# Kernel optimization log

Measured on AMD Instinct MI355X. Metric: run time of the kernel, lower is better.

The kernel has to match this reference:

```python
import jax, jax.numpy as jnp
import numpy as np

B, T = 512, 64
STOCH, DETER, HIDDEN = 32, 512, 512
ACT_DIM, EMBED = 12, 1024
MIN_STD = 0.1
LN_EPS = 1e-3


def _ln(x, g, b):
    m = x.mean(-1, keepdims=True)
    v = ((x - m) ** 2).mean(-1, keepdims=True)
    return (x - m) / jnp.sqrt(v + LN_EPS) * g + b


def setup_inputs() -> dict:
    key = jax.random.key(0)
    ks = jax.random.split(key, 12)

    def w(k, shape):
        fan_in = shape[0]
        return jax.random.normal(k, shape, jnp.float32) / np.sqrt(fan_in)

    is_first = jnp.zeros((B, T), jnp.float32).at[:, 0].set(1.0)
    return {
        "embed": jax.random.normal(ks[0], (B, T, EMBED), jnp.float32),
        "action": jax.random.normal(ks[1], (B, T, ACT_DIM), jnp.float32),
        "is_first": is_first,
        "eps_prior": jax.random.normal(ks[2], (B, T, STOCH), jnp.float32),
        "eps_post": jax.random.normal(ks[3], (B, T, STOCH), jnp.float32),
        "W_init": jax.random.normal(ks[4], (1, DETER), jnp.float32) * 0.02,
        "w_in": w(ks[5], (STOCH + ACT_DIM, HIDDEN)),
        "ln_in_g": jnp.ones((HIDDEN,), jnp.float32),
        "ln_in_b": jnp.zeros((HIDDEN,), jnp.float32),
        "w_gru": w(ks[6], (HIDDEN + DETER, 3 * DETER)),
        "ln_gru_g": jnp.ones((3 * DETER,), jnp.float32),
        "ln_gru_b": jnp.zeros((3 * DETER,), jnp.float32),
        "w_out": w(ks[7], (DETER, HIDDEN)),
        "ln_out_g": jnp.ones((HIDDEN,), jnp.float32),
        "ln_out_b": jnp.zeros((HIDDEN,), jnp.float32),
        "w_ims": w(ks[8], (HIDDEN, 2 * STOCH)),
        "b_ims": jnp.zeros((2 * STOCH,), jnp.float32),
        "w_obs": w(ks[9], (DETER + EMBED, HIDDEN)),
        "ln_obs_g": jnp.ones((HIDDEN,), jnp.float32),
        "ln_obs_b": jnp.zeros((HIDDEN,), jnp.float32),
        "w_ostat": w(ks[10], (HIDDEN, 2 * STOCH)),
        "b_ostat": jnp.zeros((2 * STOCH,), jnp.float32),
    }


def reference(embed, action, is_first, eps_prior, eps_post, W_init,
              w_in, ln_in_g, ln_in_b, w_gru, ln_gru_g, ln_gru_b,
              w_out, ln_out_g, ln_out_b, w_ims, b_ims,
              w_obs, ln_obs_g, ln_obs_b, w_ostat, b_ostat):
    # RSSM.observe with continuous stoch (discrete=False), mean_act='none',
    # std_act='softplus', initial='learned', rec_depth=1.
    def img_out_stats(deter):
        x = jax.nn.silu(_ln(deter @ w_out, ln_out_g, ln_out_b))
        s = x @ w_ims + b_ims
        mean = s[..., :STOCH]
        std = jax.nn.softplus(s[..., STOCH:]) + MIN_STD
        return mean, std

    bsz = embed.shape[0]
    deter0 = jnp.broadcast_to(jnp.tanh(W_init), (bsz, DETER))
    stoch0, _ = img_out_stats(deter0)  # mode of Normal = mean

    # time-major for scan
    eT = jnp.swapaxes(embed, 0, 1)
    aT = jnp.swapaxes(action, 0, 1)
    fT = jnp.swapaxes(is_first, 0, 1)[..., None]
    epT = jnp.swapaxes(eps_prior, 0, 1)
    eoT = jnp.swapaxes(eps_post, 0, 1)

    def step(carry, xs):
        stoch, deter = carry
        a, e, f, ep, eo = xs
        # is_first reset (blend with learned initial state)
        a = a * (1.0 - f)
        stoch = stoch * (1.0 - f) + stoch0 * f
        deter = deter * (1.0 - f) + deter0 * f
        # img_step
        x = jax.nn.silu(_ln(jnp.concatenate([stoch, a], -1) @ w_in, ln_in_g, ln_in_b))
        parts = _ln(jnp.concatenate([x, deter], -1) @ w_gru, ln_gru_g, ln_gru_b)
        r, c, u = jnp.split(parts, 3, -1)
        r = jax.nn.sigmoid(r)
        c = jnp.tanh(r * c)
        u = jax.nn.sigmoid(u - 1.0)  # update_bias = -1
        deter_n = u * c + (1.0 - u) * deter
        pm, ps = img_out_stats(deter_n)
        pstoch = pm + ps * ep  # reparameterized sample
        # obs_step posterior
        xo = jax.nn.silu(_ln(jnp.concatenate([deter_n, e], -1) @ w_obs, ln_obs_g, ln_obs_b))
        so = xo @ w_ostat + b_ostat
        om = so[..., :STOCH]
        ostd = jax.nn.softplus(so[..., STOCH:]) + MIN_STD
        ostoch = om + ostd * eo
        return (ostoch, deter_n), (ostoch, om, ostd, pstoch, pm, ps, deter_n)

    _, ys = jax.lax.scan(step, (stoch0, deter0), (aT, eT, fT, epT, eoT))
    # batch-major, concat post(stoch,mean,std) prior(stoch,mean,std) deter -> [B,T,6*STOCH+DETER]
    return jnp.concatenate([jnp.swapaxes(y, 0, 1) for y in ys], -1)
```

## Files before the change

### kernel.cpp

```cpp
#include <hip/hip_runtime.h>
#include <hip/hip_bf16.h>


typedef __attribute__((ext_vector_type(8))) short bf16x8;
typedef __attribute__((ext_vector_type(4))) float f32x4;

static __device__ __forceinline__ short f2b(float x){
  __hip_bfloat16 h = __float2bfloat16(x);
  return *reinterpret_cast<short*>(&h);
}
static __device__ __forceinline__ float b2f(short s){
  __hip_bfloat16 h = *reinterpret_cast<__hip_bfloat16*>(&s);
  return __bfloat162float(h);
}
static __device__ __forceinline__ float softplusf_(float x){
  return (x > 20.f) ? x : log1pf(expf(x));
}

static __device__ __forceinline__ float bsum(float v, float* red){
  int tid = threadIdx.x;
  __syncthreads();
  red[tid] = v; __syncthreads();
  for(int s = blockDim.x>>1; s>0; s>>=1){
    if(tid < s) red[tid] += red[tid+s];
    __syncthreads();
  }
  return red[0];
}

static __device__ __forceinline__ void stage8f(short* dst, const float* src){
  float4 f0 = *reinterpret_cast<const float4*>(src);
  float4 f1 = *reinterpret_cast<const float4*>(src+4);
  bf16x8 v;
  v[0]=f2b(f0.x); v[1]=f2b(f0.y); v[2]=f2b(f0.z); v[3]=f2b(f0.w);
  v[4]=f2b(f1.x); v[5]=f2b(f1.y); v[6]=f2b(f1.z); v[7]=f2b(f1.w);
  *reinterpret_cast<bf16x8*>(dst) = v;
}

__global__ __launch_bounds__(256) void k_wt(const float* __restrict__ wg,
    const float* __restrict__ wo, const float* __restrict__ wou,
    short* __restrict__ wgruT, short* __restrict__ wobsDT,
    short* __restrict__ wobsET, short* __restrict__ woutT){
  int i = blockIdx.x*256 + threadIdx.x;
  if(i < 1572864){ int n = i>>10, k = i&1023; wgruT[i] = f2b(wg[k*1536+n]); return; }
  i -= 1572864;
  if(i < 262144){ int n = i>>9, k = i&511; wobsDT[i] = f2b(wo[k*512+n]); return; }
  i -= 262144;
  if(i < 524288){ int n = i>>10, k = i&1023; wobsET[i] = f2b(wo[(512+k)*512+n]); return; }
  i -= 524288;
  { int n = i>>9, k = i&511; woutT[i] = f2b(wou[k*512+n]); }
}

__global__ __launch_bounds__(512) void k_init(const float* __restrict__ W_init,
    const float* __restrict__ w_out, const float* __restrict__ og, const float* __restrict__ ob,
    const float* __restrict__ w_ims, const float* __restrict__ b_ims,
    float* __restrict__ deter0, float* __restrict__ stoch0){
  __shared__ float d0[512]; __shared__ float red[512]; __shared__ float x2[512];
  int tid = threadIdx.x;
  float d = tanhf(W_init[tid]); d0[tid] = d; deter0[tid] = d; __syncthreads();
  float s = 0.f;
  for(int k=0;k<512;k++) s += d0[k]*w_out[k*512+tid];
  float sum = bsum(s, red);
  float sq  = bsum(s*s, red);
  float mu = sum/512.f, var = sq/512.f - mu*mu;
  float rstd = rsqrtf(var + 1e-3f);
  float xn = (s-mu)*rstd*og[tid] + ob[tid];
  float xs = xn/(1.f+expf(-xn));
  x2[tid] = xs; __syncthreads();
  if(tid < 32){
    float acc = b_ims[tid];
    for(int k=0;k<512;k++) acc += x2[k]*w_ims[k*64+tid];
    stoch0[tid] = acc;
  }
}

__global__ __launch_bounds__(256) void k_x0(const float* __restrict__ action,
    const float* __restrict__ is_first, const float* __restrict__ w_in,
    const float* __restrict__ ig, const float* __restrict__ ib,
    const float* __restrict__ deter0, const float* __restrict__ stoch0,
    short* __restrict__ xdeter, float* __restrict__ deterF){
  int b = blockIdx.x, tid = threadIdx.x;
  __shared__ float st[32]; __shared__ float al[12]; __shared__ float red[256];
  float f0 = is_first[b*64];
  if(tid < 32) st[tid] = stoch0[tid];
  if(tid < 12) al[tid] = action[b*768 + tid]*(1.f-f0);
  __syncthreads();
  float xp[2];
  for(int i=0;i<2;i++){
    int h = tid + i*256; float a = 0.f;
    for(int k=0;k<32;k++) a += st[k]*w_in[k*512+h];
    for(int k=0;k<12;k++) a += al[k]*w_in[(32+k)*512+h];
    xp[i] = a;
  }
  float sum = bsum(xp[0]+xp[1], red);
  float sq  = bsum(xp[0]*xp[0]+xp[1]*xp[1], red);
  float mu = sum/512.f, var = sq/512.f - mu*mu;
  float rstd = rsqrtf(var + 1e-3f);
  for(int i=0;i<2;i++){
    int h = tid + i*256;
    float xn = (xp[i]-mu)*rstd*ig[h]+ib[h];
    float xs = xn/(1.f+expf(-xn));
    xdeter[b*1024 + h] = f2b(xs);
    xdeter[b*1024 + 512 + h] = f2b(deter0[h]);
    deterF[b*512 + h] = deter0[h];
  }
}

__global__ __launch_bounds__(256) void k_gru(const short* __restrict__ Axd,
    const short* __restrict__ Bw, float* __restrict__ Cp){
  __shared__ __align__(16) short As[64][72];
  __shared__ __align__(16) short Bs[64][72];
  int tid = threadIdx.x, lane = tid&63, wid = tid>>6;
  int wm = (wid>>1)*32, wn = (wid&1)*32;
  int mP = blockIdx.x*64, nP = blockIdx.y*64;
  f32x4 acc[2][2] = {};
  for(int kt=0; kt<1024; kt+=64){
    #pragma unroll
    for(int c=0;c<2;c++){
      int idx = tid + c*256; int r = idx>>3, kc = (idx&7)*8;
      *(int4*)&As[r][kc] = *(const int4*)&Axd[(mP+r)*1024 + kt + kc];
      *(int4*)&Bs[r][kc] = *(const int4*)&Bw[(nP+r)*1024 + kt + kc];
    }
    __syncthreads();
    #pragma unroll
    for(int ks=0; ks<64; ks+=32){
      int ko = ks + 8*(lane>>4);
      bf16x8 a0 = *(const bf16x8*)&As[wm +      (lane&15)][ko];
      bf16x8 a1 = *(const bf16x8*)&As[wm + 16 + (lane&15)][ko];
      bf16x8 b0 = *(const bf16x8*)&Bs[wn +      (lane&15)][ko];
      bf16x8 b1 = *(const bf16x8*)&Bs[wn + 16 + (lane&15)][ko];
      acc[0][0] = __builtin_amdgcn_mfma_f32_16x16x32_bf16(a0,b0,acc[0][0],0,0,0);
      acc[0][1] = __builtin_amdgcn_mfma_f32_16x16x32_bf16(a0,b1,acc[0][1],0,0,0);
      acc[1][0] = __builtin_amdgcn_mfma_f32_16x16x32_bf16(a1,b0,acc[1][0],0,0,0);
      acc[1][1] = __builtin_amdgcn_mfma_f32_16x16x32_bf16(a1,b1,acc[1][1],0,0,0);
    }
    __syncthreads();
  }
  int r0 = (lane>>4)*4, c0 = lane&15;
  for(int mi=0;mi<2;mi++) for(int ni=0;ni<2;ni++){
    int row = mP + wm + mi*16 + r0, col = nP + wn + ni*16 + c0;
    #pragma unroll
    for(int r=0;r<4;r++) Cp[(row+r)*1536 + col] = acc[mi][ni][r];
  }
}

__global__ __launch_bounds__(256) void k_gates(const float* __restrict__ parts,
    const float* __restrict__ gg, const float* __restrict__ gb,
    const float* __restrict__ is_first, const float* __restrict__ deter0,
    float* __restrict__ deterF, short* __restrict__ deterB,
    float* __restrict__ out, int t){
  int b = blockIdx.x, tid = threadIdx.x;
  __shared__ float red[256];
  const float* p = parts + b*1536;
  float v[6]; float s=0.f, sq=0.f;
  #pragma unroll
  for(int k=0;k<6;k++){ v[k] = p[tid + k*256]; s += v[k]; sq += v[k]*v[k]; }
  float sum = bsum(s, red);
  float ssq = bsum(sq, red);
  float mu = sum/1536.f, var = ssq/1536.f - mu*mu;
  float rstd = rsqrtf(var + 1e-3f);
  float f = is_first[b*64 + t];
  for(int jj=0;jj<2;jj++){
    int j = tid + jj*256;
    float xr = (v[jj]  -mu)*rstd*gg[j]       + gb[j];
    float xc = (v[2+jj]-mu)*rstd*gg[512+j]   + gb[512+j];
    float xu = (v[4+jj]-mu)*rstd*gg[1024+j]  + gb[1024+j];
    float r = 1.f/(1.f+expf(-xr));
    float c = tanhf(r*xc);
    float u = 1.f/(1.f+expf(-(xu-1.f)));
    float dp = deterF[b*512+j]*(1.f-f) + deter0[j]*f;
    float dn = u*c + (1.f-u)*dp;
    deterF[b*512+j] = dn;
    deterB[b*512+j] = f2b(dn);
    out[b*45056 + t*704 + 192 + j] = dn;
  }
}

__global__ __launch_bounds__(256) void k_obs(const short* __restrict__ dB,
    const float* __restrict__ emb, const short* __restrict__ WdT,
    const short* __restrict__ WeT, float* __restrict__ xopre, int t){
  __shared__ __align__(16) short As[64][72];
  __shared__ __align__(16) short Bs[64][72];
  int tid = threadIdx.x, lane = tid&63, wid = tid>>6;
  int wm = (wid>>1)*32, wn = (wid&1)*32;
  int mP = blockIdx.x*64, nP = blockIdx.y*64;
  f32x4 acc[2][2] = {};
  for(int kt=0; kt<24; kt++){
    #pragma unroll
    for(int c=0;c<2;c++){
      int idx = tid + c*256; int r = idx>>3, kc = (idx&7)*8;
      if(kt < 8){
        *(int4*)&As[r][kc] = *(const int4*)&dB[(mP+r)*512 + kt*64 + kc];
        *(int4*)&Bs[r][kc] = *(const int4*)&WdT[(nP+r)*512 + kt*64 + kc];
      } else {
        stage8f(&As[r][kc], &emb[(mP+r)*65536 + t*1024 + (kt-8)*64 + kc]);
        *(int4*)&Bs[r][kc] = *(const int4*)&WeT[(nP+r)*1024 + (kt-8)*64 + kc];
      }
    }
    __syncthreads();
    #pragma unroll
    for(int ks=0; ks<64; ks+=32){
      int ko = ks + 8*(lane>>4);
      bf16x8 a0 = *(const bf16x8*)&As[wm +      (lane&15)][ko];
      bf16x8 a1 = *(const bf16x8*)&As[wm + 16 + (lane&15)][ko];
      bf16x8 b0 = *(const bf16x8*)&Bs[wn +      (lane&15)][ko];
      bf16x8 b1 = *(const bf16x8*)&Bs[wn + 16 + (lane&15)][ko];
      acc[0][0] = __builtin_amdgcn_mfma_f32_16x16x32_bf16(a0,b0,acc[0][0],0,0,0);
      acc[0][1] = __builtin_amdgcn_mfma_f32_16x16x32_bf16(a0,b1,acc[0][1],0,0,0);
      acc[1][0] = __builtin_amdgcn_mfma_f32_16x16x32_bf16(a1,b0,acc[1][0],0,0,0);
      acc[1][1] = __builtin_amdgcn_mfma_f32_16x16x32_bf16(a1,b1,acc[1][1],0,0,0);
    }
    __syncthreads();
  }
  int r0 = (lane>>4)*4, c0 = lane&15;
  for(int mi=0;mi<2;mi++) for(int ni=0;ni<2;ni++){
    int row = mP + wm + mi*16 + r0, col = nP + wn + ni*16 + c0;
    #pragma unroll
    for(int r=0;r<4;r++) xopre[(row+r)*512 + col] = acc[mi][ni][r];
  }
}

__global__ __launch_bounds__(256) void k_post(const float* __restrict__ xopre,
    const float* __restrict__ og, const float* __restrict__ ob,
    const float* __restrict__ w_ostat, const float* __restrict__ b_ostat,
    const float* __restrict__ eps_post, const float* __restrict__ is_first,
    const float* __restrict__ action, const float* __restrict__ w_in,
    const float* __restrict__ ig, const float* __restrict__ ib,
    const float* __restrict__ stoch0, const float* __restrict__ deter0,
    const float* __restrict__ deterF, short* __restrict__ xdeter,
    float* __restrict__ out, int t){
  int b = blockIdx.x, tid = threadIdx.x;
  __shared__ float red[256]; __shared__ float xo[512];
  __shared__ float psh[4][64]; __shared__ float sol[64];
  __shared__ float st[32]; __shared__ float al[12];
  float xv[2];
  for(int i=0;i<2;i++) xv[i] = xopre[b*512 + tid + i*256];
  float sum = bsum(xv[0]+xv[1], red);
  float sq  = bsum(xv[0]*xv[0]+xv[1]*xv[1], red);
  float mu = sum/512.f, var = sq/512.f - mu*mu;
  float rstd = rsqrtf(var + 1e-3f);
  for(int i=0;i<2;i++){
    int h = tid + i*256;
    float xn = (xv[i]-mu)*rstd*og[h]+ob[h];
    xo[h] = xn/(1.f+expf(-xn));
  }
  __syncthreads();
  { int p = tid>>6, n = tid&63; float a = 0.f;
    for(int k=p*128; k<p*128+128; k++) a += xo[k]*w_ostat[k*64+n];
    psh[p][n] = a; }
  __syncthreads();
  if(tid < 64) sol[tid] = psh[0][tid]+psh[1][tid]+psh[2][tid]+psh[3][tid] + b_ostat[tid];
  __syncthreads();
  float fn = (t < 63) ? is_first[b*64 + t + 1] : 0.f;
  if(tid < 32){
    float om = sol[tid];
    float osd = softplusf_(sol[32+tid]) + 0.1f;
    float eo = eps_post[(b*64+t)*32 + tid];
    float ost = om + osd*eo;
    int base = b*45056 + t*704;
    out[base+tid] = ost; out[base+32+tid] = om; out[base+64+tid] = osd;
    st[tid] = ost*(1.f-fn) + stoch0[tid]*fn;
  }
  if(tid < 12 && t < 63) al[tid] = action[(b*64+t+1)*12 + tid]*(1.f-fn);
  __syncthreads();
  if(t < 63){
    float xp[2];
    for(int i=0;i<2;i++){
      int h = tid + i*256; float a = 0.f;
      for(int k=0;k<32;k++) a += st[k]*w_in[k*512+h];
      for(int k=0;k<12;k++) a += al[k]*w_in[(32+k)*512+h];
      xp[i] = a;
    }
    float s2 = bsum(xp[0]+xp[1], red);
    float q2 = bsum(xp[0]*xp[0]+xp[1]*xp[1], red);
    float mu2 = s2/512.f, var2 = q2/512.f - mu2*mu2;
    float rstd2 = rsqrtf(var2 + 1e-3f);
    for(int i=0;i<2;i++){
      int h = tid + i*256;
      float xn = (xp[i]-mu2)*rstd2*ig[h]+ib[h];
      float xs = xn/(1.f+expf(-xn));
      xdeter[b*1024 + h] = f2b(xs);
      xdeter[b*1024 + 512 + h] = f2b(deterF[b*512+h]*(1.f-fn) + deter0[h]*fn);
    }
  }
}

__global__ __launch_bounds__(256) void k_img(const float* __restrict__ outp,
    const short* __restrict__ WoT, short* __restrict__ x2pre){
  __shared__ __align__(16) short As[128][72];
  __shared__ __align__(16) short Bs[128][72];
  int tid = threadIdx.x, lane = tid&63, wid = tid>>6;
  int wm = (wid>>1)*64, wn = (wid&1)*64;
  int mP = blockIdx.x*128, nP = blockIdx.y*128;
  f32x4 acc[4][4] = {};
  for(int kt=0; kt<512; kt+=64){
    #pragma unroll
    for(int c=0;c<4;c++){
      int idx = tid + c*256; int r = idx>>3, kc = (idx&7)*8;
      stage8f(&As[r][kc], &outp[(mP+r)*704 + 192 + kt + kc]);
      *(int4*)&Bs[r][kc] = *(const int4*)&WoT[(nP+r)*512 + kt + kc];
    }
    __syncthreads();
    #pragma unroll
    for(int ks=0; ks<64; ks+=32){
      int ko = ks + 8*(lane>>4);
      bf16x8 a[4], b[4];
      #pragma unroll
      for(int i=0;i<4;i++){
        a[i] = *(const bf16x8*)&As[wm + i*16 + (lane&15)][ko];
        b[i] = *(const bf16x8*)&Bs[wn + i*16 + (lane&15)][ko];
      }
      #pragma unroll
      for(int mi=0;mi<4;mi++)
        #pragma unroll
        for(int ni=0;ni<4;ni++)
          acc[mi][ni] = __builtin_amdgcn_mfma_f32_16x16x32_bf16(a[mi],b[ni],acc[mi][ni],0,0,0);
    }
    __syncthreads();
  }
  int r0 = (lane>>4)*4, c0 = lane&15;
  for(int mi=0;mi<4;mi++) for(int ni=0;ni<4;ni++){
    int row = mP + wm + mi*16 + r0, col = nP + wn + ni*16 + c0;
    #pragma unroll
    for(int r=0;r<4;r++) x2pre[(row+r)*512 + col] = f2b(acc[mi][ni][r]);
  }
}

__global__ __launch_bounds__(256) void k_imgpost(const short* __restrict__ x2pre,
    const float* __restrict__ og, const float* __restrict__ ob,
    const float* __restrict__ w_ims, const float* __restrict__ b_ims,
    const float* __restrict__ eps_prior, float* __restrict__ out){
  int tid = threadIdx.x;
  int g = tid>>5, l = tid&31;
  int rbase = blockIdx.x*8;
  __shared__ float x2[8][512]; __shared__ float sl[8][64];
  int row = rbase + g;
  float vals[16]; float s=0.f, sq=0.f;
  #pragma unroll
  for(int i=0;i<16;i++){
    int k = l + i*32;
    float v = b2f(x2pre[row*512+k]);
    vals[i] = v; s += v; sq += v*v;
  }
  #pragma unroll
  for(int m=1;m<32;m<<=1){ s += __shfl_xor(s, m); sq += __shfl_xor(sq, m); }
  float mu = s/512.f, var = sq/512.f - mu*mu;
  float rstd = rsqrtf(var + 1e-3f);
  #pragma unroll
  for(int i=0;i<16;i++){
    int k = l + i*32;
    float xn = (vals[i]-mu)*rstd*og[k]+ob[k];
    x2[g][k] = xn/(1.f+expf(-xn));
  }
  __syncthreads();
  { int q = tid>>6, n = tid&63;
    float a0=0.f, a1=0.f;
    for(int k=0;k<512;k++){
      float w = w_ims[k*64+n];
      a0 += x2[q][k]*w; a1 += x2[q+4][k]*w;
    }
    sl[q][n]=a0; sl[q+4][n]=a1; }
  __syncthreads();
  { int r = tid>>5, n = tid&31; int rw = rbase + r;
    float pm = sl[r][n] + b_ims[n];
    float psd = softplusf_(sl[r][n+32] + b_ims[n+32]) + 0.1f;
    float ep = eps_prior[rw*32+n];
    int base = rw*704;
    out[base+96+n] = pm + psd*ep; out[base+128+n] = pm; out[base+160+n] = psd; }
}

extern "C" void kernel_launch(void* const* d_in, const int* in_sizes, int n_in,
                              void* d_out, int out_size, void* d_ws, size_t ws_size,
                              hipStream_t stream) {
  const float* embed     = (const float*)d_in[0];
  const float* action    = (const float*)d_in[1];
  const float* is_first  = (const float*)d_in[2];
  const float* eps_prior = (const float*)d_in[3];
  const float* eps_post  = (const float*)d_in[4];
  const float* W_init    = (const float*)d_in[5];
  const float* w_in      = (const float*)d_in[6];
  const float* ln_in_g   = (const float*)d_in[7];
  const float* ln_in_b   = (const float*)d_in[8];
  const float* w_gru     = (const float*)d_in[9];
  const float* ln_gru_g  = (const float*)d_in[10];
  const float* ln_gru_b  = (const float*)d_in[11];
  const float* w_out     = (const float*)d_in[12];
  const float* ln_out_g  = (const float*)d_in[13];
  const float* ln_out_b  = (const float*)d_in[14];
  const float* w_ims     = (const float*)d_in[15];
  const float* b_ims     = (const float*)d_in[16];
  const float* w_obs     = (const float*)d_in[17];
  const float* ln_obs_g  = (const float*)d_in[18];
  const float* ln_obs_b  = (const float*)d_in[19];
  const float* w_ostat   = (const float*)d_in[20];
  const float* b_ostat   = (const float*)d_in[21];
  float* out = (float*)d_out;
  char* ws = (char*)d_ws;

  short* wgruT  = (short*)(ws + 0);
  short* wobsDT = (short*)(ws + 3145728);
  short* wobsET = (short*)(ws + 3670016);
  short* woutT  = (short*)(ws + 4718592);
  float* deter0 = (float*)(ws + 5242880);
  float* stoch0 = (float*)(ws + 5244928);
  short* xdeter = (short*)(ws + 5245184);
  float* parts  = (float*)(ws + 6293760);
  float* deterF = (float*)(ws + 9439488);
  short* deterB = (short*)(ws + 10488064);
  float* xopre  = (float*)(ws + 11012352);
  short* x2pre  = (short*)(ws + 12060928);

  dim3 blk(256);
  hipLaunchKernelGGL(k_wt, dim3(10240), blk, 0, stream,
                     w_gru, w_obs, w_out, wgruT, wobsDT, wobsET, woutT);
  hipLaunchKernelGGL(k_init, dim3(1), dim3(512), 0, stream,
                     W_init, w_out, ln_out_g, ln_out_b, w_ims, b_ims, deter0, stoch0);
  hipLaunchKernelGGL(k_x0, dim3(512), blk, 0, stream,
                     action, is_first, w_in, ln_in_g, ln_in_b, deter0, stoch0, xdeter, deterF);
  for(int t=0; t<64; t++){
    hipLaunchKernelGGL(k_gru, dim3(8,24), blk, 0, stream, xdeter, wgruT, parts);
    hipLaunchKernelGGL(k_gates, dim3(512), blk, 0, stream,
                       parts, ln_gru_g, ln_gru_b, is_first, deter0, deterF, deterB, out, t);
    hipLaunchKernelGGL(k_obs, dim3(8,8), blk, 0, stream,
                       deterB, embed, wobsDT, wobsET, xopre, t);
    hipLaunchKernelGGL(k_post, dim3(512), blk, 0, stream,
                       xopre, ln_obs_g, ln_obs_b, w_ostat, b_ostat, eps_post, is_first,
                       action, w_in, ln_in_g, ln_in_b, stoch0, deter0, deterF, xdeter, out, t);
  }
  hipLaunchKernelGGL(k_img, dim3(256,4), blk, 0, stream, out, woutT, x2pre);
  hipLaunchKernelGGL(k_imgpost, dim3(4096), blk, 0, stream,
                     x2pre, ln_out_g, ln_out_b, w_ims, b_ims, eps_prior, out);
}
```

Baseline: 5.789 ms.

## Fuse the whole recurrent scan into one persistent kernel with fragment-swizzled weights

The 64-step loop of four kernels per step (GRU GEMM, gates, obs GEMM, posterior plus next input) becomes one persistent kernel. It runs 32 blocks of 1024 threads, and each block owns 16 batch rows across all timesteps, keeping deter, stoch and intermediates in LDS. The input, GRU, obs and ostat weights are pre-transposed into bf16 MFMA fragment order so each wave can load B fragments straight from global memory. Layer-norm statistics use wave shuffles plus LDS atomics. The aim is to remove per-step launch overhead and the global round trips of intermediates. In exchange only 32 CUs are used, and every block re-streams several MB of weights from cache each step. Some pre-norm intermediates are also rounded to bf16.

```diff
diff --git a/kernel.cpp b/kernel.cpp
--- a/kernel.cpp
+++ b/kernel.cpp
@@ -16,39 +16,45 @@
 static __device__ __forceinline__ float softplusf_(float x){
   return (x > 20.f) ? x : log1pf(expf(x));
 }
-
-static __device__ __forceinline__ float bsum(float v, float* red){
-  int tid = threadIdx.x;
-  __syncthreads();
-  red[tid] = v; __syncthreads();
-  for(int s = blockDim.x>>1; s>0; s>>=1){
-    if(tid < s) red[tid] += red[tid+s];
-    __syncthreads();
-  }
-  return red[0];
-}
-
-static __device__ __forceinline__ void stage8f(short* dst, const float* src){
-  float4 f0 = *reinterpret_cast<const float4*>(src);
-  float4 f1 = *reinterpret_cast<const float4*>(src+4);
-  bf16x8 v;
-  v[0]=f2b(f0.x); v[1]=f2b(f0.y); v[2]=f2b(f0.z); v[3]=f2b(f0.w);
-  v[4]=f2b(f1.x); v[5]=f2b(f1.y); v[6]=f2b(f1.z); v[7]=f2b(f1.w);
-  *reinterpret_cast<bf16x8*>(dst) = v;
-}
-
-__global__ __launch_bounds__(256) void k_wt(const float* __restrict__ wg,
-    const float* __restrict__ wo, const float* __restrict__ wou,
-    short* __restrict__ wgruT, short* __restrict__ wobsDT,
-    short* __restrict__ wobsET, short* __restrict__ woutT){
+static __device__ __forceinline__ float sigm(float x){ return 1.f/(1.f+expf(-x)); }
+
+__global__ __launch_bounds__(256) void k_wt(
+    const float* __restrict__ wi, const float* __restrict__ wg,
+    const float* __restrict__ wo, const float* __restrict__ wst,
+    const float* __restrict__ wou,
+    short* __restrict__ WinT, short* __restrict__ WgruT,
+    short* __restrict__ WobsT, short* __restrict__ WostatT,
+    short* __restrict__ WoutT){
   int i = blockIdx.x*256 + threadIdx.x;
-  if(i < 1572864){ int n = i>>10, k = i&1023; wgruT[i] = f2b(wg[k*1536+n]); return; }
+  if(i < 32768){
+    int e=i&7, l=(i>>3)&63, f=i>>9; int ks=f&1, nt=f>>1;
+    int k=ks*32+((l>>4))*8+e, n=nt*16+(l&15);
+    WinT[i] = (k<44)? f2b(wi[k*512+n]) : (short)0;
+    return;
+  }
+  i -= 32768;
+  if(i < 1572864){
+    int e=i&7, l=(i>>3)&63, f=i>>9; int ks=f&31, nt=f>>5;
+    int k=ks*32+((l>>4))*8+e, n=nt*16+(l&15);
+    WgruT[i] = f2b(wg[k*1536+n]);
+    return;
+  }
   i -= 1572864;
-  if(i < 262144){ int n = i>>9, k = i&511; wobsDT[i] = f2b(wo[k*512+n]); return; }
-  i -= 262144;
-  if(i < 524288){ int n = i>>10, k = i&1023; wobsET[i] = f2b(wo[(512+k)*512+n]); return; }
-  i -= 524288;
-  { int n = i>>9, k = i&511; woutT[i] = f2b(wou[k*512+n]); }
+  if(i < 786432){
+    int e=i&7, l=(i>>3)&63, f=i>>9; int ks=f%48, nt=f/48;
+    int k=ks*32+((l>>4))*8+e, n=nt*16+(l&15);
+    WobsT[i] = f2b(wo[k*512+n]);
+    return;
+  }
+  i -= 786432;
+  if(i < 32768){
+    int e=i&7, l=(i>>3)&63, f=i>>9; int ks=f&15, nt=f>>4;
+    int k=ks*32+((l>>4))*8+e, n=nt*16+(l&15);
+    WostatT[i] = f2b(wst[k*64+n]);
+    return;
+  }
+  i -= 32768;
+  { int n=i>>9, k=i&511; WoutT[i] = f2b(wou[k*512+n]); }
 }
 
 __global__ __launch_bounds__(512) void k_init(const float* __restrict__ W_init,
@@ -60,12 +66,16 @@
   float d = tanhf(W_init[tid]); d0[tid] = d; deter0[tid] = d; __syncthreads();
   float s = 0.f;
   for(int k=0;k<512;k++) s += d0[k]*w_out[k*512+tid];
-  float sum = bsum(s, red);
-  float sq  = bsum(s*s, red);
+  red[tid] = s; __syncthreads();
+  for(int ss=256; ss>0; ss>>=1){ if(tid<ss) red[tid]+=red[tid+ss]; __syncthreads(); }
+  float sum = red[0]; __syncthreads();
+  red[tid] = s*s; __syncthreads();
+  for(int ss=256; ss>0; ss>>=1){ if(tid<ss) red[tid]+=red[tid+ss]; __syncthreads(); }
+  float sq = red[0];
   float mu = sum/512.f, var = sq/512.f - mu*mu;
   float rstd = rsqrtf(var + 1e-3f);
   float xn = (s-mu)*rstd*og[tid] + ob[tid];
-  float xs = xn/(1.f+expf(-xn));
+  float xs = xn*sigm(xn);
   x2[tid] = xs; __syncthreads();
   if(tid < 32){
     float acc = b_ims[tid];
@@ -74,214 +84,257 @@
   }
 }
 
-__global__ __launch_bounds__(256) void k_x0(const float* __restrict__ action,
-    const float* __restrict__ is_first, const float* __restrict__ w_in,
-    const float* __restrict__ ig, const float* __restrict__ ib,
+__global__ __launch_bounds__(1024, 4) void k_scan(
+    const float* __restrict__ embed, const float* __restrict__ action,
+    const float* __restrict__ isf, const float* __restrict__ eps_post,
+    const short* __restrict__ WinT, const float* __restrict__ ig, const float* __restrict__ ib,
+    const short* __restrict__ WgruT, const float* __restrict__ gg, const float* __restrict__ gb,
+    const short* __restrict__ WobsT, const float* __restrict__ og, const float* __restrict__ ob,
+    const short* __restrict__ WostatT, const float* __restrict__ b_ostat,
     const float* __restrict__ deter0, const float* __restrict__ stoch0,
-    short* __restrict__ xdeter, float* __restrict__ deterF){
-  int b = blockIdx.x, tid = threadIdx.x;
-  __shared__ float st[32]; __shared__ float al[12]; __shared__ float red[256];
-  float f0 = is_first[b*64];
-  if(tid < 32) st[tid] = stoch0[tid];
-  if(tid < 12) al[tid] = action[b*768 + tid]*(1.f-f0);
+    float* __restrict__ out)
+{
+  __shared__ __align__(16) short RB[16*1544];
+  __shared__ float deterS[16][516];
+  __shared__ short dB[16][520];
+  __shared__ short xrow[16][72];
+  __shared__ float stochS[16][32];
+  __shared__ float sol[16][64];
+  __shared__ float sumA[16], sqA[16];
+  __shared__ float fr[16];
+  __shared__ float d0s[512]; __shared__ float s0s[32];
+
+  const int g = blockIdx.x, tid = threadIdx.x;
+  const int w = tid>>6, lane = tid&63;
+  const int col0 = lane&15, rg4 = (lane>>4)*4;
+  float* xoF = (float*)RB;
+
+  if(tid < 512) d0s[tid] = deter0[tid];
+  if(tid < 32)  s0s[tid] = stoch0[tid];
   __syncthreads();
-  float xp[2];
-  for(int i=0;i<2;i++){
-    int h = tid + i*256; float a = 0.f;
-    for(int k=0;k<32;k++) a += st[k]*w_in[k*512+h];
-    for(int k=0;k<12;k++) a += al[k]*w_in[(32+k)*512+h];
-    xp[i] = a;
-  }
-  float sum = bsum(xp[0]+xp[1], red);
-  float sq  = bsum(xp[0]*xp[0]+xp[1]*xp[1], red);
-  float mu = sum/512.f, var = sq/512.f - mu*mu;
-  float rstd = rsqrtf(var + 1e-3f);
-  for(int i=0;i<2;i++){
-    int h = tid + i*256;
-    float xn = (xp[i]-mu)*rstd*ig[h]+ib[h];
-    float xs = xn/(1.f+expf(-xn));
-    xdeter[b*1024 + h] = f2b(xs);
-    xdeter[b*1024 + 512 + h] = f2b(deter0[h]);
-    deterF[b*512 + h] = deter0[h];
-  }
-}
-
-__global__ __launch_bounds__(256) void k_gru(const short* __restrict__ Axd,
-    const short* __restrict__ Bw, float* __restrict__ Cp){
-  __shared__ __align__(16) short As[64][72];
-  __shared__ __align__(16) short Bs[64][72];
-  int tid = threadIdx.x, lane = tid&63, wid = tid>>6;
-  int wm = (wid>>1)*32, wn = (wid&1)*32;
-  int mP = blockIdx.x*64, nP = blockIdx.y*64;
-  f32x4 acc[2][2] = {};
-  for(int kt=0; kt<1024; kt+=64){
+  { int r = tid>>6, kb = (tid&63)*8;
     #pragma unroll
-    for(int c=0;c<2;c++){
-      int idx = tid + c*256; int r = idx>>3, kc = (idx&7)*8;
-      *(int4*)&As[r][kc] = *(const int4*)&Axd[(mP+r)*1024 + kt + kc];
-      *(int4*)&Bs[r][kc] = *(const int4*)&Bw[(nP+r)*1024 + kt + kc];
-    }
-    __syncthreads();
-    #pragma unroll
-    for(int ks=0; ks<64; ks+=32){
-      int ko = ks + 8*(lane>>4);
-      bf16x8 a0 = *(const bf16x8*)&As[wm +      (lane&15)][ko];
-      bf16x8 a1 = *(const bf16x8*)&As[wm + 16 + (lane&15)][ko];
-      bf16x8 b0 = *(const bf16x8*)&Bs[wn +      (lane&15)][ko];
-      bf16x8 b1 = *(const bf16x8*)&Bs[wn + 16 + (lane&15)][ko];
-      acc[0][0] = __builtin_amdgcn_mfma_f32_16x16x32_bf16(a0,b0,acc[0][0],0,0,0);
-      acc[0][1] = __builtin_amdgcn_mfma_f32_16x16x32_bf16(a0,b1,acc[0][1],0,0,0);
-      acc[1][0] = __builtin_amdgcn_mfma_f32_16x16x32_bf16(a1,b0,acc[1][0],0,0,0);
-      acc[1][1] = __builtin_amdgcn_mfma_f32_16x16x32_bf16(a1,b1,acc[1][1],0,0,0);
-    }
-    __syncthreads();
-  }
-  int r0 = (lane>>4)*4, c0 = lane&15;
-  for(int mi=0;mi<2;mi++) for(int ni=0;ni<2;ni++){
-    int row = mP + wm + mi*16 + r0, col = nP + wn + ni*16 + c0;
-    #pragma unroll
-    for(int r=0;r<4;r++) Cp[(row+r)*1536 + col] = acc[mi][ni][r];
-  }
-}
-
-__global__ __launch_bounds__(256) void k_gates(const float* __restrict__ parts,
-    const float* __restrict__ gg, const float* __restrict__ gb,
-    const float* __restrict__ is_first, const float* __restrict__ deter0,
-    float* __restrict__ deterF, short* __restrict__ deterB,
-    float* __restrict__ out, int t){
-  int b = blockIdx.x, tid = threadIdx.x;
-  __shared__ float red[256];
-  const float* p = parts + b*1536;
-  float v[6]; float s=0.f, sq=0.f;
-  #pragma unroll
-  for(int k=0;k<6;k++){ v[k] = p[tid + k*256]; s += v[k]; sq += v[k]*v[k]; }
-  float sum = bsum(s, red);
-  float ssq = bsum(sq, red);
-  float mu = sum/1536.f, var = ssq/1536.f - mu*mu;
-  float rstd = rsqrtf(var + 1e-3f);
-  float f = is_first[b*64 + t];
-  for(int jj=0;jj<2;jj++){
-    int j = tid + jj*256;
-    float xr = (v[jj]  -mu)*rstd*gg[j]       + gb[j];
-    float xc = (v[2+jj]-mu)*rstd*gg[512+j]   + gb[512+j];
-    float xu = (v[4+jj]-mu)*rstd*gg[1024+j]  + gb[1024+j];
-    float r = 1.f/(1.f+expf(-xr));
-    float c = tanhf(r*xc);
-    float u = 1.f/(1.f+expf(-(xu-1.f)));
-    float dp = deterF[b*512+j]*(1.f-f) + deter0[j]*f;
-    float dn = u*c + (1.f-u)*dp;
-    deterF[b*512+j] = dn;
-    deterB[b*512+j] = f2b(dn);
-    out[b*45056 + t*704 + 192 + j] = dn;
-  }
-}
-
-__global__ __launch_bounds__(256) void k_obs(const short* __restrict__ dB,
-    const float* __restrict__ emb, const short* __restrict__ WdT,
-    const short* __restrict__ WeT, float* __restrict__ xopre, int t){
-  __shared__ __align__(16) short As[64][72];
-  __shared__ __align__(16) short Bs[64][72];
-  int tid = threadIdx.x, lane = tid&63, wid = tid>>6;
-  int wm = (wid>>1)*32, wn = (wid&1)*32;
-  int mP = blockIdx.x*64, nP = blockIdx.y*64;
-  f32x4 acc[2][2] = {};
-  for(int kt=0; kt<24; kt++){
-    #pragma unroll
-    for(int c=0;c<2;c++){
-      int idx = tid + c*256; int r = idx>>3, kc = (idx&7)*8;
-      if(kt < 8){
-        *(int4*)&As[r][kc] = *(const int4*)&dB[(mP+r)*512 + kt*64 + kc];
-        *(int4*)&Bs[r][kc] = *(const int4*)&WdT[(nP+r)*512 + kt*64 + kc];
-      } else {
-        stage8f(&As[r][kc], &emb[(mP+r)*65536 + t*1024 + (kt-8)*64 + kc]);
-        *(int4*)&Bs[r][kc] = *(const int4*)&WeT[(nP+r)*1024 + (kt-8)*64 + kc];
-      }
-    }
-    __syncthreads();
-    #pragma unroll
-    for(int ks=0; ks<64; ks+=32){
-      int ko = ks + 8*(lane>>4);
-      bf16x8 a0 = *(const bf16x8*)&As[wm +      (lane&15)][ko];
-      bf16x8 a1 = *(const bf16x8*)&As[wm + 16 + (lane&15)][ko];
-      bf16x8 b0 = *(const bf16x8*)&Bs[wn +      (lane&15)][ko];
-      bf16x8 b1 = *(const bf16x8*)&Bs[wn + 16 + (lane&15)][ko];
-      acc[0][0] = __builtin_amdgcn_mfma_f32_16x16x32_bf16(a0,b0,acc[0][0],0,0,0);
-      acc[0][1] = __builtin_amdgcn_mfma_f32_16x16x32_bf16(a0,b1,acc[0][1],0,0,0);
-      acc[1][0] = __builtin_amdgcn_mfma_f32_16x16x32_bf16(a1,b0,acc[1][0],0,0,0);
-      acc[1][1] = __builtin_amdgcn_mfma_f32_16x16x32_bf16(a1,b1,acc[1][1],0,0,0);
-    }
-    __syncthreads();
-  }
-  int r0 = (lane>>4)*4, c0 = lane&15;
-  for(int mi=0;mi<2;mi++) for(int ni=0;ni<2;ni++){
-    int row = mP + wm + mi*16 + r0, col = nP + wn + ni*16 + c0;
-    #pragma unroll
-    for(int r=0;r<4;r++) xopre[(row+r)*512 + col] = acc[mi][ni][r];
-  }
-}
-
-__global__ __launch_bounds__(256) void k_post(const float* __restrict__ xopre,
-    const float* __restrict__ og, const float* __restrict__ ob,
-    const float* __restrict__ w_ostat, const float* __restrict__ b_ostat,
-    const float* __restrict__ eps_post, const float* __restrict__ is_first,
-    const float* __restrict__ action, const float* __restrict__ w_in,
-    const float* __restrict__ ig, const float* __restrict__ ib,
-    const float* __restrict__ stoch0, const float* __restrict__ deter0,
-    const float* __restrict__ deterF, short* __restrict__ xdeter,
-    float* __restrict__ out, int t){
-  int b = blockIdx.x, tid = threadIdx.x;
-  __shared__ float red[256]; __shared__ float xo[512];
-  __shared__ float psh[4][64]; __shared__ float sol[64];
-  __shared__ float st[32]; __shared__ float al[12];
-  float xv[2];
-  for(int i=0;i<2;i++) xv[i] = xopre[b*512 + tid + i*256];
-  float sum = bsum(xv[0]+xv[1], red);
-  float sq  = bsum(xv[0]*xv[0]+xv[1]*xv[1], red);
-  float mu = sum/512.f, var = sq/512.f - mu*mu;
-  float rstd = rsqrtf(var + 1e-3f);
-  for(int i=0;i<2;i++){
-    int h = tid + i*256;
-    float xn = (xv[i]-mu)*rstd*og[h]+ob[h];
-    xo[h] = xn/(1.f+expf(-xn));
-  }
+    for(int i=0;i<8;i++) deterS[r][kb+i] = d0s[kb+i]; }
+  if(tid < 512){ int r=tid>>5, c=tid&31; stochS[r][c] = s0s[c]; }
   __syncthreads();
-  { int p = tid>>6, n = tid&63; float a = 0.f;
-    for(int k=p*128; k<p*128+128; k++) a += xo[k]*w_ostat[k*64+n];
-    psh[p][n] = a; }
-  __syncthreads();
-  if(tid < 64) sol[tid] = psh[0][tid]+psh[1][tid]+psh[2][tid]+psh[3][tid] + b_ostat[tid];
-  __syncthreads();
-  float fn = (t < 63) ? is_first[b*64 + t + 1] : 0.f;
-  if(tid < 32){
-    float om = sol[tid];
-    float osd = softplusf_(sol[32+tid]) + 0.1f;
-    float eo = eps_post[(b*64+t)*32 + tid];
-    float ost = om + osd*eo;
-    int base = b*45056 + t*704;
-    out[base+tid] = ost; out[base+32+tid] = om; out[base+64+tid] = osd;
-    st[tid] = ost*(1.f-fn) + stoch0[tid]*fn;
-  }
-  if(tid < 12 && t < 63) al[tid] = action[(b*64+t+1)*12 + tid]*(1.f-fn);
-  __syncthreads();
-  if(t < 63){
-    float xp[2];
-    for(int i=0;i<2;i++){
-      int h = tid + i*256; float a = 0.f;
-      for(int k=0;k<32;k++) a += st[k]*w_in[k*512+h];
-      for(int k=0;k<12;k++) a += al[k]*w_in[(32+k)*512+h];
-      xp[i] = a;
-    }
-    float s2 = bsum(xp[0]+xp[1], red);
-    float q2 = bsum(xp[0]*xp[0]+xp[1]*xp[1], red);
-    float mu2 = s2/512.f, var2 = q2/512.f - mu2*mu2;
-    float rstd2 = rsqrtf(var2 + 1e-3f);
-    for(int i=0;i<2;i++){
-      int h = tid + i*256;
-      float xn = (xp[i]-mu2)*rstd2*ig[h]+ib[h];
-      float xs = xn/(1.f+expf(-xn));
-      xdeter[b*1024 + h] = f2b(xs);
-      xdeter[b*1024 + 512 + h] = f2b(deterF[b*512+h]*(1.f-fn) + deter0[h]*fn);
-    }
+
+  for(int t=0; t<64; t++){
+    if(tid < 16){ fr[tid] = isf[(g*16+tid)*64 + t]; sumA[tid]=0.f; sqA[tid]=0.f; }
+    __syncthreads();
+    if(tid < 512){
+      int r = tid>>5, c = tid&31; float f = fr[r];
+      float sm = stochS[r][c]*(1.f-f) + s0s[c]*f;
+      xrow[r][c] = f2b(sm);
+      if(c < 12){
+        float av = action[((size_t)(g*16+r)*64+t)*12 + c]*(1.f-f);
+        xrow[r][32+c] = f2b(av);
+      }
+      if(c >= 12) xrow[r][32+c] = 0;
+    }
+    { int r = tid>>6, kb = (tid&63)*8; float f = fr[r];
+      #pragma unroll
+      for(int i=0;i<8;i++){
+        int k = kb+i;
+        float dm = deterS[r][k]*(1.f-f) + d0s[k]*f;
+        deterS[r][k] = dm;
+        RB[r*1032 + 512 + k] = f2b(dm);
+      } }
+    __syncthreads();
+    {
+      f32x4 acc[2] = {};
+      #pragma unroll
+      for(int ks=0; ks<2; ks++){
+        bf16x8 a = *(const bf16x8*)&xrow[col0][ks*32 + (lane>>4)*8];
+        #pragma unroll
+        for(int j=0;j<2;j++){
+          int nt = w*2+j;
+          bf16x8 b = *(const bf16x8*)&WinT[((nt*2 + ks)*64 + lane)*8];
+          acc[j] = __builtin_amdgcn_mfma_f32_16x16x32_bf16(a,b,acc[j],0,0,0);
+        }
+      }
+      float s[4]={0,0,0,0}, q[4]={0,0,0,0};
+      #pragma unroll
+      for(int j=0;j<2;j++){
+        int col = (w*2+j)*16 + col0;
+        #pragma unroll
+        for(int r=0;r<4;r++){
+          float v = acc[j][r];
+          RB[(rg4+r)*1032 + col] = f2b(v);
+          s[r]+=v; q[r]+=v*v;
+        }
+      }
+      #pragma unroll
+      for(int r=0;r<4;r++){
+        #pragma unroll
+        for(int m=1;m<16;m<<=1){ s[r]+=__shfl_xor(s[r],m); q[r]+=__shfl_xor(q[r],m); }
+      }
+      if(col0==0){
+        #pragma unroll
+        for(int r=0;r<4;r++){ atomicAdd(&sumA[rg4+r], s[r]); atomicAdd(&sqA[rg4+r], q[r]); }
+      }
+    }
+    __syncthreads();
+    {
+      int r = tid>>6, kb = tid&63;
+      float mu = sumA[r]/512.f, var = sqA[r]/512.f - mu*mu;
+      float rstd = rsqrtf(var + 1e-3f);
+      #pragma unroll
+      for(int i=0;i<8;i++){
+        int k = kb + i*64;
+        float v = b2f(RB[r*1032 + k]);
+        float xn = (v-mu)*rstd*ig[k] + ib[k];
+        RB[r*1032 + k] = f2b(xn*sigm(xn));
+      }
+    }
+    __syncthreads();
+    {
+      if(tid < 16){ sumA[tid]=0.f; sqA[tid]=0.f; }
+      f32x4 acc[6] = {};
+      const short* xdA = &RB[col0*1032 + (lane>>4)*8];
+      for(int ks=0; ks<32; ks++){
+        bf16x8 a = *(const bf16x8*)(xdA + ks*32);
+        #pragma unroll
+        for(int j=0;j<6;j++){
+          bf16x8 b = *(const bf16x8*)&WgruT[((size_t)((w*6+j)*32 + ks)*64 + lane)*8];
+          acc[j] = __builtin_amdgcn_mfma_f32_16x16x32_bf16(a,b,acc[j],0,0,0);
+        }
+      }
+      __syncthreads();
+      float s[4]={0,0,0,0}, q[4]={0,0,0,0};
+      #pragma unroll
+      for(int j=0;j<6;j++){
+        int col = (w*6+j)*16 + col0;
+        #pragma unroll
+        for(int r=0;r<4;r++){
+          float v = acc[j][r];
+          RB[(rg4+r)*1544 + col] = f2b(v);
+          s[r]+=v; q[r]+=v*v;
+        }
+      }
+      #pragma unroll
+      for(int r=0;r<4;r++){
+        #pragma unroll
+        for(int m=1;m<16;m<<=1){ s[r]+=__shfl_xor(s[r],m); q[r]+=__shfl_xor(q[r],m); }
+      }
+      if(col0==0){
+        #pragma unroll
+        for(int r=0;r<4;r++){ atomicAdd(&sumA[rg4+r], s[r]); atomicAdd(&sqA[rg4+r], q[r]); }
+      }
+    }
+    __syncthreads();
+    {
+      int r = tid>>6, jb = tid&63;
+      float mu = sumA[r]/1536.f, var = sqA[r]/1536.f - mu*mu;
+      float rstd = rsqrtf(var + 1e-3f);
+      size_t obase = (size_t)(g*16+r)*45056 + (size_t)t*704 + 192;
+      #pragma unroll
+      for(int i=0;i<8;i++){
+        int j = jb + i*64;
+        float xr = (b2f(RB[r*1544 + j      ])-mu)*rstd*gg[j]      + gb[j];
+        float xc = (b2f(RB[r*1544 + 512 + j])-mu)*rstd*gg[512+j]  + gb[512+j];
+        float xu = (b2f(RB[r*1544 + 1024+ j])-mu)*rstd*gg[1024+j] + gb[1024+j];
+        float rr = sigm(xr);
+        float cc = tanhf(rr*xc);
+        float uu = sigm(xu-1.f);
+        float dp = deterS[r][j];
+        float dn = uu*cc + (1.f-uu)*dp;
+        deterS[r][j] = dn;
+        dB[r][j] = f2b(dn);
+        out[obase + j] = dn;
+      }
+    }
+    __syncthreads();
+    if(tid < 16){ sumA[tid]=0.f; sqA[tid]=0.f; }
+    {
+      int r = tid>>6, kb = (tid&63)*16;
+      const float4* ep = (const float4*)&embed[((size_t)(g*16+r)*64+t)*1024 + kb];
+      #pragma unroll
+      for(int v4=0; v4<4; v4++){
+        float4 e = ep[v4];
+        RB[r*1032 + kb + v4*4 + 0] = f2b(e.x);
+        RB[r*1032 + kb + v4*4 + 1] = f2b(e.y);
+        RB[r*1032 + kb + v4*4 + 2] = f2b(e.z);
+        RB[r*1032 + kb + v4*4 + 3] = f2b(e.w);
+      }
+    }
+    __syncthreads();
+    {
+      f32x4 acc[2] = {};
+      for(int ks=0; ks<16; ks++){
+        bf16x8 a = *(const bf16x8*)&dB[col0][ks*32 + (lane>>4)*8];
+        #pragma unroll
+        for(int j=0;j<2;j++){
+          bf16x8 b = *(const bf16x8*)&WobsT[((size_t)((w*2+j)*48 + ks)*64 + lane)*8];
+          acc[j] = __builtin_amdgcn_mfma_f32_16x16x32_bf16(a,b,acc[j],0,0,0);
+        }
+      }
+      for(int ks=16; ks<48; ks++){
+        bf16x8 a = *(const bf16x8*)&RB[col0*1032 + (ks-16)*32 + (lane>>4)*8];
+        #pragma unroll
+        for(int j=0;j<2;j++){
+          bf16x8 b = *(const bf16x8*)&WobsT[((size_t)((w*2+j)*48 + ks)*64 + lane)*8];
+          acc[j] = __builtin_amdgcn_mfma_f32_16x16x32_bf16(a,b,acc[j],0,0,0);
+        }
+      }
+      __syncthreads();
+      float s[4]={0,0,0,0}, q[4]={0,0,0,0};
+      #pragma unroll
+      for(int j=0;j<2;j++){
+        int col = (w*2+j)*16 + col0;
+        #pragma unroll
+        for(int r=0;r<4;r++){
+          float v = acc[j][r];
+          xoF[(rg4+r)*520 + col] = v;
+          s[r]+=v; q[r]+=v*v;
+        }
+      }
+      #pragma unroll
+      for(int r=0;r<4;r++){
+        #pragma unroll
+        for(int m=1;m<16;m<<=1){ s[r]+=__shfl_xor(s[r],m); q[r]+=__shfl_xor(q[r],m); }
+      }
+      if(col0==0){
+        #pragma unroll
+        for(int r=0;r<4;r++){ atomicAdd(&sumA[rg4+r], s[r]); atomicAdd(&sqA[rg4+r], q[r]); }
+      }
+    }
+    __syncthreads();
+    {
+      int r = tid>>6, kb = tid&63;
+      float mu = sumA[r]/512.f, var = sqA[r]/512.f - mu*mu;
+      float rstd = rsqrtf(var + 1e-3f);
+      #pragma unroll
+      for(int i=0;i<8;i++){
+        int k = kb + i*64;
+        float v = xoF[r*520 + k];
+        float xn = (v-mu)*rstd*og[k] + ob[k];
+        dB[r][k] = f2b(xn*sigm(xn));
+      }
+    }
+    __syncthreads();
+    if(w < 4){
+      f32x4 acc = {};
+      for(int ks=0; ks<16; ks++){
+        bf16x8 a = *(const bf16x8*)&dB[col0][ks*32 + (lane>>4)*8];
+        bf16x8 b = *(const bf16x8*)&WostatT[((w*16 + ks)*64 + lane)*8];
+        acc = __builtin_amdgcn_mfma_f32_16x16x32_bf16(a,b,acc,0,0,0);
+      }
+      #pragma unroll
+      for(int r=0;r<4;r++) sol[rg4+r][w*16+col0] = acc[r];
+    }
+    __syncthreads();
+    if(tid < 512){
+      int r = tid>>5, c = tid&31;
+      float om  = sol[r][c]    + b_ostat[c];
+      float spi = sol[r][32+c] + b_ostat[32+c];
+      float osd = softplusf_(spi) + 0.1f;
+      float eo  = eps_post[((size_t)(g*16+r)*64+t)*32 + c];
+      float ost = om + osd*eo;
+      size_t base = (size_t)(g*16+r)*45056 + (size_t)t*704;
+      out[base+c] = ost; out[base+32+c] = om; out[base+64+c] = osd;
+      stochS[r][c] = ost;
+    }
+    __syncthreads();
   }
 }
 
@@ -297,7 +350,13 @@
     #pragma unroll
     for(int c=0;c<4;c++){
       int idx = tid + c*256; int r = idx>>3, kc = (idx&7)*8;
-      stage8f(&As[r][kc], &outp[(mP+r)*704 + 192 + kt + kc]);
+      const float* src = &outp[(size_t)(mP+r)*704 + 192 + kt + kc];
+      float4 f0 = *reinterpret_cast<const float4*>(src);
+      float4 f1 = *reinterpret_cast<const float4*>(src+4);
+      bf16x8 v;
+      v[0]=f2b(f0.x); v[1]=f2b(f0.y); v[2]=f2b(f0.z); v[3]=f2b(f0.w);
+      v[4]=f2b(f1.x); v[5]=f2b(f1.y); v[6]=f2b(f1.z); v[7]=f2b(f1.w);
+      *reinterpret_cast<bf16x8*>(&As[r][kc]) = v;
       *(int4*)&Bs[r][kc] = *(const int4*)&WoT[(nP+r)*512 + kt + kc];
     }
     __syncthreads();
@@ -322,7 +381,7 @@
   for(int mi=0;mi<4;mi++) for(int ni=0;ni<4;ni++){
     int row = mP + wm + mi*16 + r0, col = nP + wn + ni*16 + c0;
     #pragma unroll
-    for(int r=0;r<4;r++) x2pre[(row+r)*512 + col] = f2b(acc[mi][ni][r]);
+    for(int r=0;r<4;r++) x2pre[(size_t)(row+r)*512 + col] = f2b(acc[mi][ni][r]);
   }
 }
 
@@ -339,7 +398,7 @@
   #pragma unroll
   for(int i=0;i<16;i++){
     int k = l + i*32;
-    float v = b2f(x2pre[row*512+k]);
+    float v = b2f(x2pre[(size_t)row*512+k]);
     vals[i] = v; s += v; sq += v*v;
   }
   #pragma unroll
@@ -364,8 +423,8 @@
   { int r = tid>>5, n = tid&31; int rw = rbase + r;
     float pm = sl[r][n] + b_ims[n];
     float psd = softplusf_(sl[r][n+32] + b_ims[n+32]) + 0.1f;
-    float ep = eps_prior[rw*32+n];
-    int base = rw*704;
+    float ep = eps_prior[(size_t)rw*32+n];
+    size_t base = (size_t)rw*704;
     out[base+96+n] = pm + psd*ep; out[base+128+n] = pm; out[base+160+n] = psd; }
 }
 
@@ -397,37 +456,29 @@
   float* out = (float*)d_out;
   char* ws = (char*)d_ws;
 
-  short* wgruT  = (short*)(ws + 0);
-  short* wobsDT = (short*)(ws + 3145728);
-  short* wobsET = (short*)(ws + 3670016);
-  short* woutT  = (short*)(ws + 4718592);
-  float* deter0 = (float*)(ws + 5242880);
-  float* stoch0 = (float*)(ws + 5244928);
-  short* xdeter = (short*)(ws + 5245184);
-  float* parts  = (float*)(ws + 6293760);
-  float* deterF = (float*)(ws + 9439488);
-  short* deterB = (short*)(ws + 10488064);
-  float* xopre  = (float*)(ws + 11012352);
-  short* x2pre  = (short*)(ws + 12060928);
+  short* WinT    = (short*)(ws + 0);
+  short* WgruT   = (short*)(ws + 65536);
+  short* WobsT   = (short*)(ws + 3211264);
+  short* WostatT = (short*)(ws + 4784128);
+  short* WoutT   = (short*)(ws + 4849664);
+  float* deter0  = (float*)(ws + 5373952);
+  float* stoch0  = (float*)(ws + 5376000);
+  short* x2pre   = (short*)(ws + 5376256);
 
   dim3 blk(256);
-  hipLaunchKernelGGL(k_wt, dim3(10240), blk, 0, stream,
-                     w_gru, w_obs, w_out, wgruT, wobsDT, wobsET, woutT);
+  hipLaunchKernelGGL(k_wt, dim3(10496), blk, 0, stream,
+                     w_in, w_gru, w_obs, w_ostat, w_out,
+                     WinT, WgruT, WobsT, WostatT, WoutT);
   hipLaunchKernelGGL(k_init, dim3(1), dim3(512), 0, stream,
                      W_init, w_out, ln_out_g, ln_out_b, w_ims, b_ims, deter0, stoch0);
-  hipLaunchKernelGGL(k_x0, dim3(512), blk, 0, stream,
-                     action, is_first, w_in, ln_in_g, ln_in_b, deter0, stoch0, xdeter, deterF);
-  for(int t=0; t<64; t++){
-    hipLaunchKernelGGL(k_gru, dim3(8,24), blk, 0, stream, xdeter, wgruT, parts);
-    hipLaunchKernelGGL(k_gates, dim3(512), blk, 0, stream,
-                       parts, ln_gru_g, ln_gru_b, is_first, deter0, deterF, deterB, out, t);
-    hipLaunchKernelGGL(k_obs, dim3(8,8), blk, 0, stream,
-                       deterB, embed, wobsDT, wobsET, xopre, t);
-    hipLaunchKernelGGL(k_post, dim3(512), blk, 0, stream,
-                       xopre, ln_obs_g, ln_obs_b, w_ostat, b_ostat, eps_post, is_first,
-                       action, w_in, ln_in_g, ln_in_b, stoch0, deter0, deterF, xdeter, out, t);
-  }
-  hipLaunchKernelGGL(k_img, dim3(256,4), blk, 0, stream, out, woutT, x2pre);
+  hipLaunchKernelGGL(k_scan, dim3(32), dim3(1024), 0, stream,
+                     embed, action, is_first, eps_post,
+                     WinT, ln_in_g, ln_in_b,
+                     WgruT, ln_gru_g, ln_gru_b,
+                     WobsT, ln_obs_g, ln_obs_b,
+                     WostatT, b_ostat,
+                     deter0, stoch0, out);
+  hipLaunchKernelGGL(k_img, dim3(256,4), blk, 0, stream, out, WoutT, x2pre);
   hipLaunchKernelGGL(k_imgpost, dim3(4096), blk, 0, stream,
                      x2pre, ln_out_g, ln_out_b, w_ims, b_ims, eps_prior, out);
 }
```

Measured after the change: 8.561 ms. +47.9%, slower.
